# Optimization experiments

Hardware: AMD Instinct MI355X
Metric: run time of the kernel (lower is better)

The kernel has to match this reference:

```python
import jax, jax.numpy as jnp
import numpy as np

N = 50000  # nodes == edges (source multiplies [N,H] node tensor by [E] edge attention)
HW = 8


def _adaptive_pool_2x2_from9(h):
    # PyTorch AdaptiveAvgPool2d((2,2)) on 9x9: bins [0:5) and [4:9) per dim (overlap at 4)
    def binpair(t, ax):
        s0 = jnp.take(t, jnp.arange(0, 5), axis=ax).mean(axis=ax)
        s1 = jnp.take(t, jnp.arange(4, 9), axis=ax).mean(axis=ax)
        return jnp.stack([s0, s1], axis=ax)
    return binpair(binpair(h, 3), 2)  # [N,64,2,2]


def _fe_net(x, c1w, c1b, c2w, c2b, fw, fb):
    h = x[:, None, :, :]  # [N,1,8,8]
    h = jax.lax.conv_general_dilated(h, c1w, (1, 1), ((1, 1), (1, 1)),
                                     dimension_numbers=('NCHW', 'OIHW', 'NCHW')) + c1b[None, :, None, None]
    h = jax.nn.relu(h)  # [N,32,8,8]
    h = jax.lax.conv_general_dilated(h, c2w, (1, 1), ((1, 1), (1, 1)),
                                     dimension_numbers=('NCHW', 'OIHW', 'NCHW')) + c2b[None, :, None, None]
    h = jax.nn.relu(h)  # [N,64,9,9]
    h = _adaptive_pool_2x2_from9(h).reshape(h.shape[0], -1)  # [N,256]
    return h @ fw + fb  # [N,32]


def _gcn(x, src, dst, W, b, n):
    h = x @ W
    idx = jnp.arange(n)
    s = jnp.concatenate([src, idx])
    d = jnp.concatenate([dst, idx])
    deg = jax.ops.segment_sum(jnp.ones(s.shape[0], h.dtype), d, num_segments=n)
    dis = jnp.where(deg > 0, jax.lax.rsqrt(jnp.maximum(deg, 1e-12)), 0.0)
    norm = dis[s] * dis[d]
    out = jax.ops.segment_sum(h[s] * norm[:, None], d, num_segments=n)
    return out + b


def _attention1(aux, src, dst, n):
    frame = aux[:, 2]
    fd = jnp.abs(frame[src] - frame[dst])
    outdeg = jax.ops.segment_sum(jnp.ones(src.shape[0], aux.dtype), src, num_segments=n)
    return jnp.where(fd == 1.0, 1.0 / jnp.maximum(outdeg[src], 1.0), 0.0)


def _attention2(aux, src, dst):
    ang, rad, frame = aux[:, 0], aux[:, 1], aux[:, 2]
    fd = jnp.abs(frame[src] - frame[dst])
    dx = rad[dst] * jnp.cos(ang[dst]) - rad[src] * jnp.cos(ang[src])
    dy = rad[dst] * jnp.sin(ang[dst]) - rad[src] * jnp.sin(ang[src])
    fd_safe = jnp.where(fd == 2.0, fd, 1.0)
    vel = jnp.sqrt(dx * dx + dy * dy + 1e-12) / fd_safe
    return jnp.where(fd == 2.0, jnp.exp(-vel / 8.5), 0.0)


def setup_inputs() -> dict:
    key = jax.random.key(0)
    ks = jax.random.split(key, 20)
    x = jax.random.normal(ks[0], (N, HW, HW), jnp.float32)
    angle = jax.random.uniform(ks[1], (N,), jnp.float32, 0.0, 2.0 * np.pi)
    radius = jax.random.uniform(ks[2], (N,), jnp.float32, 1.0, 100.0)
    frame = jax.random.randint(ks[3], (N,), 0, 10).astype(jnp.float32)
    aux_features = jnp.stack([angle, radius, frame], axis=1)
    edge_index = jax.random.randint(ks[4], (2, N), 0, N)
    s = 0.05
    p = lambda k, sh: jax.random.normal(k, sh, jnp.float32) * s
    return {
        'x': x, 'aux_features': aux_features, 'edge_index': edge_index,
        'conv1_w': p(ks[5], (32, 1, 3, 3)), 'conv1_b': jnp.zeros((32,), jnp.float32),
        'conv2_w': p(ks[6], (64, 32, 2, 2)), 'conv2_b': jnp.zeros((64,), jnp.float32),
        'fe_fc_w': p(ks[7], (256, 32)), 'fe_fc_b': jnp.zeros((32,), jnp.float32),
        'gcn1_w': p(ks[8], (32, 64)), 'gcn1_b': jnp.zeros((64,), jnp.float32),
        'gcn2_w': p(ks[9], (64, 64)), 'gcn2_b': jnp.zeros((64,), jnp.float32),
        'fc_w': p(ks[10], (64, 32)), 'fc_b': jnp.zeros((32,), jnp.float32),
        'out_w': p(ks[11], (32, 1)), 'out_b': jnp.zeros((1,), jnp.float32),
    }


def reference(x, aux_features, edge_index, conv1_w, conv1_b, conv2_w, conv2_b,
              fe_fc_w, fe_fc_b, gcn1_w, gcn1_b, gcn2_w, gcn2_b, fc_w, fc_b,
              out_w, out_b):
    n = x.shape[0]
    src, dst = edge_index[0], edge_index[1]
    sig = _fe_net(x, conv1_w, conv1_b, conv2_w, conv2_b, fe_fc_w, fe_fc_b)  # [N,32]
    att1 = _attention1(aux_features, src, dst, n)  # [E] == [N]
    x1 = jax.nn.relu(_gcn(sig, src, dst, gcn1_w, gcn1_b, n) * att1[:, None])
    att2 = _attention2(aux_features, src, dst)
    x2 = jax.nn.relu(_gcn(x1, src, dst, gcn2_w, gcn2_b, n) * att2[:, None])
    h = jax.nn.relu(x2 @ fc_w + fc_b)
    out = jax.nn.sigmoid(h @ out_w + out_b)  # [N,1]
    return out
```

## Files before the change

### kernel.cpp

```cpp
#include <hip/hip_runtime.h>
#include <math.h>

typedef float f32x4 __attribute__((ext_vector_type(4)));
typedef float f32x2 __attribute__((ext_vector_type(2)));
typedef __bf16 bf16x8 __attribute__((ext_vector_type(8)));
typedef unsigned short ushort8 __attribute__((ext_vector_type(8)));
typedef unsigned short ushort4v __attribute__((ext_vector_type(4)));

static __device__ __forceinline__ unsigned short bfbits(float f) {
    return __builtin_bit_cast(unsigned short, (__bf16)f);
}

__global__ __launch_bounds__(256, 3) void fe_kernel(
    const float* __restrict__ x,
    const float* __restrict__ w1T,
    const float* __restrict__ w2, const float* __restrict__ b2,
    unsigned short* __restrict__ poolbf, int n)
{
    __shared__ unsigned short hT[4][100][40];
    __shared__ float xs[4][104];

    const int t = threadIdx.x, lane = t & 63, wave = t >> 6;
    const int cl = lane & 15, kg = lane >> 4;

    bf16x8 bfr[4][4];
    #pragma unroll
    for (int ct = 0; ct < 4; ++ct)
        #pragma unroll
        for (int tap = 0; tap < 4; ++tap) {
            const float* gp = w2 + (size_t)(ct * 16 + cl) * 128 + kg * 32 + tap;
            ushort8 u;
            #pragma unroll
            for (int e = 0; e < 8; ++e) u[e] = bfbits(gp[e * 4]);
            bfr[ct][tap] = __builtin_bit_cast(bf16x8, u);
        }
    float b2r[4];
    #pragma unroll
    for (int ct = 0; ct < 4; ++ct) b2r[ct] = b2[ct * 16 + cl];

    unsigned int pm[3] = {0u, 0u, 0u};
    #pragma unroll
    for (int mt = 0; mt < 6; ++mt)
        #pragma unroll
        for (int rg = 0; rg < 4; ++rg) {
            const int slot = mt * 4 + rg;
            const int pd = mt * 16 + kg * 4 + rg;
            unsigned int bits = 0;
            if (pd < 81) {
                const int id = pd / 9, jd = pd - 9 * (pd / 9);
                if (id <= 4 && jd <= 4) bits |= 1u;
                if (id <= 4 && jd >= 4) bits |= 2u;
                if (id >= 4 && jd <= 4) bits |= 4u;
                if (id >= 4 && jd >= 4) bits |= 8u;
            }
            pm[slot >> 3] |= bits << ((slot & 7) * 4);
        }

    int rbase[6];
    #pragma unroll
    for (int mt = 0; mt < 6; ++mt) {
        const int p = mt * 16 + cl;
        const int ia = p / 9, ja = p - 9 * ia;
        rbase[mt] = (p < 81) ? (ia * 10 + ja) : 0;
    }

    {
        ushort8 z8 = {0,0,0,0,0,0,0,0};
        for (int r = lane; r < 100; r += 64) {
            const int pi = r / 10, pj = r - 10 * (r / 10);
            if (pi == 0 || pi == 9 || pj == 0 || pj == 9) {
                *reinterpret_cast<ushort8*>(&hT[wave][r][0])  = z8;
                *reinterpret_cast<ushort8*>(&hT[wave][r][8])  = z8;
                *reinterpret_cast<ushort8*>(&hT[wave][r][16]) = z8;
                *reinterpret_cast<ushort8*>(&hT[wave][r][24]) = z8;
                xs[wave][r] = 0.0f;
            }
        }
    }

    const int i = lane >> 3, j = lane & 7;
    const int rr = (i + 1) * 10 + (j + 1);
    const int gw = blockIdx.x * 4 + wave;
    const int nw = gridDim.x * 4;

    float v = (gw < n) ? x[(size_t)gw * 64 + lane] : 0.0f;

    for (int node = gw; node < n; node += nw) {
        #pragma unroll
        for (int ct = 0; ct < 4; ++ct)
            #pragma unroll
            for (int tap = 0; tap < 4; ++tap) {
                f32x4 tmp = __builtin_bit_cast(f32x4, bfr[ct][tap]);
                asm volatile("" : "+v"(tmp));
                bfr[ct][tap] = __builtin_bit_cast(bf16x8, tmp);
            }

        const int nn = node + nw;
        const float vnext = x[(size_t)(nn < n ? nn : node) * 64 + lane];

        xs[wave][rr] = v;
        asm volatile("s_waitcnt lgkmcnt(0)" ::: "memory");

        float xv[9];
        #pragma unroll
        for (int ki = 0; ki < 3; ++ki)
            #pragma unroll
            for (int kj = 0; kj < 3; ++kj)
                xv[ki * 3 + kj] = xs[wave][(i + ki) * 10 + (j + kj)];

        #pragma unroll
        for (int cp = 0; cp < 4; ++cp) {
            ushort8 hv;
            #pragma unroll
            for (int half = 0; half < 2; ++half) {
                const int cg = cp * 2 + half;
                f32x4 s = *reinterpret_cast<const f32x4*>(w1T + 288 + cg * 4);
                #pragma unroll
                for (int q = 0; q < 9; ++q) {
                    const f32x4 wq = *reinterpret_cast<const f32x4*>(w1T + q * 32 + cg * 4);
                    s += xv[q] * wq;
                }
                #pragma unroll
                for (int c = 0; c < 4; ++c)
                    hv[half * 4 + c] = bfbits(fmaxf(s[c], 0.0f));
            }
            *reinterpret_cast<ushort8*>(&hT[wave][rr][cp * 8]) = hv;
        }
        asm volatile("s_waitcnt lgkmcnt(0)" ::: "memory");

        f32x2 pb01[4], pb23[4];
        #pragma unroll
        for (int ct = 0; ct < 4; ++ct) { pb01[ct] = (f32x2){0.f,0.f}; pb23[ct] = (f32x2){0.f,0.f}; }

        #pragma unroll
        for (int mt = 0; mt < 6; ++mt) {
            const int rb = rbase[mt];
            bf16x8 a[4];
            a[0] = *reinterpret_cast<const bf16x8*>(&hT[wave][rb][kg * 8]);
            a[1] = *reinterpret_cast<const bf16x8*>(&hT[wave][rb + 1][kg * 8]);
            a[2] = *reinterpret_cast<const bf16x8*>(&hT[wave][rb + 10][kg * 8]);
            a[3] = *reinterpret_cast<const bf16x8*>(&hT[wave][rb + 11][kg * 8]);

            f32x4 acc[4];
            #pragma unroll
            for (int ct = 0; ct < 4; ++ct)
                acc[ct] = (f32x4){b2r[ct], b2r[ct], b2r[ct], b2r[ct]};
            #pragma unroll
            for (int tap = 0; tap < 4; ++tap)
                #pragma unroll
                for (int ct = 0; ct < 4; ++ct)
                    acc[ct] = __builtin_amdgcn_mfma_f32_16x16x32_bf16(a[tap], bfr[ct][tap], acc[ct], 0, 0, 0);

            #pragma unroll
            for (int rg = 0; rg < 4; ++rg) {
                if (mt * 16 + rg >= 81) continue;
                const int slot = mt * 4 + rg;
                const unsigned int bits = pm[slot >> 3] >> ((slot & 7) * 4);
                const f32x2 w01 = {(float)(bits & 1u), (float)((bits >> 1) & 1u)};
                const f32x2 w23 = {(float)((bits >> 2) & 1u), (float)((bits >> 3) & 1u)};
                #pragma unroll
                for (int ct = 0; ct < 4; ++ct) {
                    const float vr = fmaxf(acc[ct][rg], 0.0f);
                    const f32x2 v2 = {vr, vr};
                    pb01[ct] += v2 * w01;
                    pb23[ct] += v2 * w23;
                }
            }
        }

        const bool k0 = (kg & 1) != 0;
        const bool k1 = (kg & 2) != 0;
        float outb[4];
        #pragma unroll
        for (int b = 0; b < 4; ++b) {
            const float x0 = (b < 2) ? pb01[0][b] : pb23[0][b - 2];
            const float x1 = (b < 2) ? pb01[1][b] : pb23[1][b - 2];
            const float x2 = (b < 2) ? pb01[2][b] : pb23[2][b - 2];
            const float x3 = (b < 2) ? pb01[3][b] : pb23[3][b - 2];
            float keepA = k0 ? x1 : x0, sendA = k0 ? x0 : x1;
            float keepB = k0 ? x3 : x2, sendB = k0 ? x2 : x3;
            keepA += __shfl_xor(sendA, 16);
            keepB += __shfl_xor(sendB, 16);
            float keep = k1 ? keepB : keepA, send = k1 ? keepA : keepB;
            keep += __shfl_xor(send, 32);
            outb[b] = keep;
        }
        ushort4v pv;
        #pragma unroll
        for (int b = 0; b < 4; ++b) pv[b] = bfbits(outb[b]);
        *reinterpret_cast<ushort4v*>(poolbf + (size_t)node * 256 + lane * 4) = pv;

        v = vnext;
    }
}

__global__ void pre_k(const float* __restrict__ fw, const float* __restrict__ fb,
                      const float* __restrict__ g1w, const float* __restrict__ g2w,
                      const float* __restrict__ w1, const float* __restrict__ b1,
                      unsigned short* __restrict__ W1t, float* __restrict__ v1,
                      unsigned short* __restrict__ W2t, float* __restrict__ w1T)
{
    const int b = blockIdx.x, t = threadIdx.x;
    if (b < 64) {
        float s = 0.0f;
        for (int jj = 0; jj < 32; ++jj) s += fw[t * 32 + jj] * g1w[jj * 64 + b];
        W1t[b * 256 + t] = bfbits(0.04f * s);
    } else if (b < 80) {
        const int idx = (b - 64) * 256 + t;
        const int nc = idx >> 6, k = idx & 63;
        W2t[nc * 64 + k] = bfbits(g2w[k * 64 + nc]);
        if (b == 64 && t < 64) {
            float s = 0.0f;
            for (int jj = 0; jj < 32; ++jj) s += fb[jj] * g1w[jj * 64 + t];
            v1[t] = s;
        }
    } else {
        if (t < 320) {
            const int q = t >> 5, c = t & 31;
            w1T[t] = (q < 9) ? w1[c * 9 + q] : b1[c];
        }
    }
}

template<int NKS, bool HASV>
__global__ __launch_bounds__(256) void mm_k(
    const unsigned short* __restrict__ A, const unsigned short* __restrict__ Bt,
    const float* __restrict__ v1, float* __restrict__ h, int n)
{
    const int lane = threadIdx.x & 63;
    const int cl = lane & 15, kg = lane >> 4;
    const int gw = blockIdx.x * 4 + (threadIdx.x >> 6);
    const int nw = gridDim.x * 4;
    const int K = NKS * 32;
    const int ntiles = (n + 15) >> 4;

    float vv[4];
    #pragma unroll
    for (int nt = 0; nt < 4; ++nt) vv[nt] = HASV ? v1[nt * 16 + cl] : 0.0f;

    for (int mt = gw; mt < ntiles; mt += nw) {
        const int r = min(mt * 16 + cl, n - 1);
        const unsigned short* ar = A + (size_t)r * K + kg * 8;
        f32x4 acc[4];
        #pragma unroll
        for (int nt = 0; nt < 4; ++nt)
            acc[nt] = (f32x4){vv[nt], vv[nt], vv[nt], vv[nt]};
        #pragma unroll
        for (int ks = 0; ks < NKS; ++ks) {
            const bf16x8 afr = *reinterpret_cast<const bf16x8*>(ar + ks * 32);
            #pragma unroll
            for (int nt = 0; nt < 4; ++nt) {
                const bf16x8 bfrg = *reinterpret_cast<const bf16x8*>(
                    Bt + (size_t)(nt * 16 + cl) * K + ks * 32 + kg * 8);
                acc[nt] = __builtin_amdgcn_mfma_f32_16x16x32_bf16(afr, bfrg, acc[nt], 0, 0, 0);
            }
        }
        #pragma unroll
        for (int nt = 0; nt < 4; ++nt)
            #pragma unroll
            for (int rg = 0; rg < 4; ++rg) {
                const int row = mt * 16 + (kg << 2) + rg;
                if (row < n) h[(size_t)row * 64 + nt * 16 + cl] = acc[nt][rg];
            }
    }
}

__global__ void count_k(const int* __restrict__ ei, float* __restrict__ outdeg,
                        float* __restrict__ indeg, int m)
{
    int e = blockIdx.x * blockDim.x + threadIdx.x;
    if (e >= m) return;
    atomicAdd(&outdeg[ei[e]], 1.0f);
    atomicAdd(&indeg[ei[m + e]], 1.0f);
}

__global__ void attprep_k(const float* __restrict__ aux, const int* __restrict__ ei,
                          const float* __restrict__ outdeg, const float* __restrict__ indeg,
                          float* __restrict__ dis,
                          float* __restrict__ att1, float* __restrict__ att2,
                          int n, int m)
{
    int e = blockIdx.x * blockDim.x + threadIdx.x;
    if (e < n) dis[e] = rsqrtf(indeg[e] + 1.0f);
    if (e >= m) return;
    const int s = ei[e], d = ei[m + e];
    const float fs = aux[(size_t)s * 3 + 2], fdd = aux[(size_t)d * 3 + 2];
    const float fd = fabsf(fs - fdd);
    att1[e] = (fd == 1.0f) ? (1.0f / fmaxf(outdeg[s], 1.0f)) : 0.0f;
    const float angs = aux[(size_t)s * 3 + 0], rads = aux[(size_t)s * 3 + 1];
    const float angd = aux[(size_t)d * 3 + 0], radd = aux[(size_t)d * 3 + 1];
    const float dx = radd * cosf(angd) - rads * cosf(angs);
    const float dy = radd * sinf(angd) - rads * sinf(angs);
    const float vel = sqrtf(dx * dx + dy * dy + 1e-12f) * 0.5f;
    att2[e] = (fd == 2.0f) ? expf(-vel / 8.5f) : 0.0f;
}

__global__ void scatter_k(const float* __restrict__ h, const int* __restrict__ ei,
                          const float* __restrict__ dis, float* __restrict__ acc, int m)
{
    size_t idx = (size_t)blockIdx.x * blockDim.x + threadIdx.x;
    if (idx >= (size_t)m * 64) return;
    const int e = (int)(idx >> 6), k = (int)(idx & 63);
    const int s = ei[e], d = ei[m + e];
    const float w = dis[s] * dis[d];
    atomicAdd(&acc[(size_t)d * 64 + k], w * h[(size_t)s * 64 + k]);
}

template<bool BF16OUT>
__global__ void fin_k(const float* __restrict__ acc, const float* __restrict__ h,
                      const float* __restrict__ dis, const float* __restrict__ b,
                      const float* __restrict__ att,
                      unsigned short* __restrict__ xbf, float* __restrict__ xf, int n)
{
    size_t idx = (size_t)blockIdx.x * blockDim.x + threadIdx.x;
    if (idx >= (size_t)n * 64) return;
    const int node = (int)(idx >> 6), k = (int)(idx & 63);
    const float di = dis[node];
    const float v = fmaxf((acc[idx] + b[k] + di * di * h[idx]) * att[node], 0.0f);
    if (BF16OUT) xbf[idx] = bfbits(v);
    else         xf[idx] = v;
}

__global__ void head_k(const float* __restrict__ x2, const float* __restrict__ fcw,
                       const float* __restrict__ fcb, const float* __restrict__ outw,
                       const float* __restrict__ outb, float* __restrict__ out, int n)
{
    size_t idx = (size_t)blockIdx.x * blockDim.x + threadIdx.x;
    const int node = (int)(idx >> 5), o = (int)(idx & 31);
    if (node >= n) return;
    const float* xr = x2 + (size_t)node * 64;
    float s = fcb[o];
    #pragma unroll
    for (int k = 0; k < 64; ++k) s = fmaf(xr[k], fcw[k * 32 + o], s);
    s = fmaxf(s, 0.0f);
    float p = s * outw[o];
    #pragma unroll
    for (int mk = 16; mk >= 1; mk >>= 1) p += __shfl_xor(p, mk);
    if (o == 0) out[node] = 1.0f / (1.0f + expf(-(p + outb[0])));
}

extern "C" void kernel_launch(void* const* d_in, const int* in_sizes, int n_in,
                              void* d_out, int out_size, void* d_ws, size_t ws_size,
                              hipStream_t stream)
{
    const float* x    = (const float*)d_in[0];
    const float* aux  = (const float*)d_in[1];
    const int*   ei   = (const int*)  d_in[2];
    const float* c1w  = (const float*)d_in[3];
    const float* c1b  = (const float*)d_in[4];
    const float* c2w  = (const float*)d_in[5];
    const float* c2b  = (const float*)d_in[6];
    const float* few  = (const float*)d_in[7];
    const float* feb  = (const float*)d_in[8];
    const float* g1w  = (const float*)d_in[9];
    const float* g1b  = (const float*)d_in[10];
    const float* g2w  = (const float*)d_in[11];
    const float* g2b  = (const float*)d_in[12];
    const float* fcw  = (const float*)d_in[13];
    const float* fcb  = (const float*)d_in[14];
    const float* outw = (const float*)d_in[15];
    const float* outb = (const float*)d_in[16];
    float* out = (float*)d_out;

    const int n = in_sizes[0] / 64;
    const int m = in_sizes[2] / 2;

    float* ws = (float*)d_ws;
    unsigned short* poolbf = (unsigned short*)ws;
    float* acc  = ws;
    unsigned short* x1bf = (unsigned short*)(ws + (size_t)n * 64);
    float* h    = ws + (size_t)n * 128;
    unsigned short* W1t = (unsigned short*)(ws + (size_t)n * 192);
    float* v1   = ws + (size_t)n * 192 + 8192;
    unsigned short* W2t = (unsigned short*)(v1 + 64);
    float* w1T    = v1 + 64 + 2048;
    float* outdeg = w1T + 320;
    float* indeg  = outdeg + n;
    float* dis    = indeg + n;
    float* att1   = dis + n;
    float* att2   = att1 + m;

    const dim3 b256(256);
    const int gE   = (m + 255) / 256;
    const int gNE  = (max(n, m) + 255) / 256;
    const int gNM  = (int)(((size_t)n * 64 + 255) / 256);
    const int gEM  = (int)(((size_t)m * 64 + 255) / 256);
    const int gNH  = (int)(((size_t)n * 32 + 255) / 256);
    const int gMM  = (((n + 15) / 16) + 3) / 4;

    hipMemsetAsync(outdeg, 0, (size_t)2 * n * sizeof(float), stream);
    pre_k<<<81, b256, 0, stream>>>(few, feb, g1w, g2w, c1w, c1b, W1t, v1, W2t, w1T);
    fe_kernel<<<768, b256, 0, stream>>>(x, w1T, c2w, c2b, poolbf, n);

    count_k<<<gE, b256, 0, stream>>>(ei, outdeg, indeg, m);
    attprep_k<<<gNE, b256, 0, stream>>>(aux, ei, outdeg, indeg, dis, att1, att2, n, m);

    mm_k<8, true><<<gMM, b256, 0, stream>>>(poolbf, W1t, v1, h, n);
    hipMemsetAsync(acc, 0, (size_t)n * 64 * sizeof(float), stream);
    scatter_k<<<gEM, b256, 0, stream>>>(h, ei, dis, acc, m);
    fin_k<true><<<gNM, b256, 0, stream>>>(acc, h, dis, g1b, att1, x1bf, nullptr, n);

    mm_k<2, false><<<gMM, b256, 0, stream>>>(x1bf, W2t, nullptr, h, n);
    hipMemsetAsync(acc, 0, (size_t)n * 64 * sizeof(float), stream);
    scatter_k<<<gEM, b256, 0, stream>>>(h, ei, dis, acc, m);
    fin_k<false><<<gNM, b256, 0, stream>>>(acc, h, dis, g2b, att2, nullptr, h, n);

    head_k<<<gNH, b256, 0, stream>>>(h, fcw, fcb, outw, outb, out, n);
}
```

Baseline: 301.0 us.

## Fuse setup, attention, finalize and head stages into fewer kernels

Degree counting is merged into the weight-prep kernel, and the attention and normalisation prep now runs on extra blocks of the first GEMM launch. The accumulator memsets are replaced by zeroing inside the GEMM kernels when the workspace is large enough. The first layer's finalize step is folded into the second GEMM's A-operand load, and the second finalize is merged with the MLP head through shared memory. This removes several launches and intermediate round trips through global memory. The cost is heavier kernels, a workspace-size-dependent layout, and in-place read and write of h and acc inside mm2f_k.

Measured after the change: 263.4 us. -12.5%, faster.

```diff
diff --git a/kernel.cpp b/kernel.cpp
--- a/kernel.cpp
+++ b/kernel.cpp
@@ -194,11 +194,13 @@
     }
 }
 
-__global__ void pre_k(const float* __restrict__ fw, const float* __restrict__ fb,
-                      const float* __restrict__ g1w, const float* __restrict__ g2w,
-                      const float* __restrict__ w1, const float* __restrict__ b1,
-                      unsigned short* __restrict__ W1t, float* __restrict__ v1,
-                      unsigned short* __restrict__ W2t, float* __restrict__ w1T)
+__global__ void precount_k(const float* __restrict__ fw, const float* __restrict__ fb,
+                           const float* __restrict__ g1w, const float* __restrict__ g2w,
+                           const float* __restrict__ w1, const float* __restrict__ b1,
+                           unsigned short* __restrict__ W1t, float* __restrict__ v1,
+                           unsigned short* __restrict__ W2t, float* __restrict__ w1T,
+                           const int* __restrict__ ei, float* __restrict__ outdeg,
+                           float* __restrict__ indeg, int m)
 {
     const int b = blockIdx.x, t = threadIdx.x;
     if (b < 64) {
@@ -214,45 +216,135 @@
             for (int jj = 0; jj < 32; ++jj) s += fb[jj] * g1w[jj * 64 + t];
             v1[t] = s;
         }
-    } else {
-        if (t < 320) {
+        if (b == 65 && t < 320) {
             const int q = t >> 5, c = t & 31;
             w1T[t] = (q < 9) ? w1[c * 9 + q] : b1[c];
         }
-    }
-}
-
-template<int NKS, bool HASV>
-__global__ __launch_bounds__(256) void mm_k(
+    } else {
+        const int e = (b - 80) * 256 + t;
+        if (e >= m) return;
+        atomicAdd(&outdeg[ei[e]], 1.0f);
+        atomicAdd(&indeg[ei[m + e]], 1.0f);
+    }
+}
+
+template<bool ZEROACC>
+__global__ __launch_bounds__(256) void mm1att_k(
     const unsigned short* __restrict__ A, const unsigned short* __restrict__ Bt,
-    const float* __restrict__ v1, float* __restrict__ h, int n)
+    const float* __restrict__ v1, float* __restrict__ h, float* __restrict__ acc,
+    const float* __restrict__ aux, const int* __restrict__ ei,
+    const float* __restrict__ outdeg, const float* __restrict__ indeg,
+    float* __restrict__ dis, float* __restrict__ att1, float* __restrict__ att2,
+    int n, int m, int gmm)
+{
+    const int t = threadIdx.x;
+    if ((int)blockIdx.x >= gmm) {
+        const int e = (blockIdx.x - gmm) * 256 + t;
+        if (e < n) dis[e] = rsqrtf(indeg[e] + 1.0f);
+        if (e >= m) return;
+        const int s = ei[e], d = ei[m + e];
+        const float fs = aux[(size_t)s * 3 + 2], fdd = aux[(size_t)d * 3 + 2];
+        const float fd = fabsf(fs - fdd);
+        att1[e] = (fd == 1.0f) ? (1.0f / fmaxf(outdeg[s], 1.0f)) : 0.0f;
+        const float angs = aux[(size_t)s * 3 + 0], rads = aux[(size_t)s * 3 + 1];
+        const float angd = aux[(size_t)d * 3 + 0], radd = aux[(size_t)d * 3 + 1];
+        const float dx = radd * cosf(angd) - rads * cosf(angs);
+        const float dy = radd * sinf(angd) - rads * sinf(angs);
+        const float vel = sqrtf(dx * dx + dy * dy + 1e-12f) * 0.5f;
+        att2[e] = (fd == 2.0f) ? expf(-vel / 8.5f) : 0.0f;
+        return;
+    }
+
+    const int lane = t & 63;
+    const int cl = lane & 15, kg = lane >> 4;
+    const int gw = blockIdx.x * 4 + (t >> 6);
+    const int nw = gmm * 4;
+    const int ntiles = (n + 15) >> 4;
+
+    float vv[4];
+    #pragma unroll
+    for (int nt = 0; nt < 4; ++nt) vv[nt] = v1[nt * 16 + cl];
+
+    for (int mt = gw; mt < ntiles; mt += nw) {
+        const int r = min(mt * 16 + cl, n - 1);
+        const unsigned short* ar = A + (size_t)r * 256 + kg * 8;
+        f32x4 accf[4];
+        #pragma unroll
+        for (int nt = 0; nt < 4; ++nt)
+            accf[nt] = (f32x4){vv[nt], vv[nt], vv[nt], vv[nt]};
+        #pragma unroll
+        for (int ks = 0; ks < 8; ++ks) {
+            const bf16x8 afr = *reinterpret_cast<const bf16x8*>(ar + ks * 32);
+            #pragma unroll
+            for (int nt = 0; nt < 4; ++nt) {
+                const bf16x8 bfrg = *reinterpret_cast<const bf16x8*>(
+                    Bt + (size_t)(nt * 16 + cl) * 256 + ks * 32 + kg * 8);
+                accf[nt] = __builtin_amdgcn_mfma_f32_16x16x32_bf16(afr, bfrg, accf[nt], 0, 0, 0);
+            }
+        }
+        #pragma unroll
+        for (int nt = 0; nt < 4; ++nt)
+            #pragma unroll
+            for (int rg = 0; rg < 4; ++rg) {
+                const int row = mt * 16 + (kg << 2) + rg;
+                if (row < n) h[(size_t)row * 64 + nt * 16 + cl] = accf[nt][rg];
+            }
+        if (ZEROACC) {
+            const int zr = mt * 16 + cl;
+            if (zr < n) {
+                const f32x4 z = {0.f, 0.f, 0.f, 0.f};
+                float* zp = acc + (size_t)zr * 64 + kg * 16;
+                *reinterpret_cast<f32x4*>(zp)      = z;
+                *reinterpret_cast<f32x4*>(zp + 4)  = z;
+                *reinterpret_cast<f32x4*>(zp + 8)  = z;
+                *reinterpret_cast<f32x4*>(zp + 12) = z;
+            }
+        }
+    }
+}
+
+template<bool ZEROACC>
+__global__ __launch_bounds__(256) void mm2f_k(
+    const float* __restrict__ acc, const float* __restrict__ hin,
+    const float* __restrict__ dis, const float* __restrict__ g1b,
+    const float* __restrict__ att1, const unsigned short* __restrict__ Bt,
+    float* __restrict__ hout, float* __restrict__ accz, int n)
 {
     const int lane = threadIdx.x & 63;
     const int cl = lane & 15, kg = lane >> 4;
     const int gw = blockIdx.x * 4 + (threadIdx.x >> 6);
     const int nw = gridDim.x * 4;
-    const int K = NKS * 32;
     const int ntiles = (n + 15) >> 4;
-
-    float vv[4];
-    #pragma unroll
-    for (int nt = 0; nt < 4; ++nt) vv[nt] = HASV ? v1[nt * 16 + cl] : 0.0f;
 
     for (int mt = gw; mt < ntiles; mt += nw) {
         const int r = min(mt * 16 + cl, n - 1);
-        const unsigned short* ar = A + (size_t)r * K + kg * 8;
-        f32x4 acc[4];
-        #pragma unroll
-        for (int nt = 0; nt < 4; ++nt)
-            acc[nt] = (f32x4){vv[nt], vv[nt], vv[nt], vv[nt]};
-        #pragma unroll
-        for (int ks = 0; ks < NKS; ++ks) {
-            const bf16x8 afr = *reinterpret_cast<const bf16x8*>(ar + ks * 32);
+        const float di = dis[r];
+        const float di2 = di * di;
+        const float at = att1[r];
+        f32x4 accf[4];
+        #pragma unroll
+        for (int nt = 0; nt < 4; ++nt) accf[nt] = (f32x4){0.f, 0.f, 0.f, 0.f};
+        #pragma unroll
+        for (int ks = 0; ks < 2; ++ks) {
+            const float* ap = acc + (size_t)r * 64 + ks * 32 + kg * 8;
+            const float* hp = hin + (size_t)r * 64 + ks * 32 + kg * 8;
+            const float* bp = g1b + ks * 32 + kg * 8;
+            ushort8 u;
+            #pragma unroll
+            for (int e = 0; e < 8; ++e)
+                u[e] = bfbits(fmaxf((ap[e] + bp[e] + di2 * hp[e]) * at, 0.0f));
+            if (ZEROACC) {
+                const f32x4 z = {0.f, 0.f, 0.f, 0.f};
+                float* zp = accz + (size_t)r * 64 + ks * 32 + kg * 8;
+                *reinterpret_cast<f32x4*>(zp)     = z;
+                *reinterpret_cast<f32x4*>(zp + 4) = z;
+            }
+            const bf16x8 afr = __builtin_bit_cast(bf16x8, u);
             #pragma unroll
             for (int nt = 0; nt < 4; ++nt) {
                 const bf16x8 bfrg = *reinterpret_cast<const bf16x8*>(
-                    Bt + (size_t)(nt * 16 + cl) * K + ks * 32 + kg * 8);
-                acc[nt] = __builtin_amdgcn_mfma_f32_16x16x32_bf16(afr, bfrg, acc[nt], 0, 0, 0);
+                    Bt + (size_t)(nt * 16 + cl) * 64 + ks * 32 + kg * 8);
+                accf[nt] = __builtin_amdgcn_mfma_f32_16x16x32_bf16(afr, bfrg, accf[nt], 0, 0, 0);
             }
         }
         #pragma unroll
@@ -260,39 +352,9 @@
             #pragma unroll
             for (int rg = 0; rg < 4; ++rg) {
                 const int row = mt * 16 + (kg << 2) + rg;
-                if (row < n) h[(size_t)row * 64 + nt * 16 + cl] = acc[nt][rg];
-            }
-    }
-}
-
-__global__ void count_k(const int* __restrict__ ei, float* __restrict__ outdeg,
-                        float* __restrict__ indeg, int m)
-{
-    int e = blockIdx.x * blockDim.x + threadIdx.x;
-    if (e >= m) return;
-    atomicAdd(&outdeg[ei[e]], 1.0f);
-    atomicAdd(&indeg[ei[m + e]], 1.0f);
-}
-
-__global__ void attprep_k(const float* __restrict__ aux, const int* __restrict__ ei,
-                          const float* __restrict__ outdeg, const float* __restrict__ indeg,
-                          float* __restrict__ dis,
-                          float* __restrict__ att1, float* __restrict__ att2,
-                          int n, int m)
-{
-    int e = blockIdx.x * blockDim.x + threadIdx.x;
-    if (e < n) dis[e] = rsqrtf(indeg[e] + 1.0f);
-    if (e >= m) return;
-    const int s = ei[e], d = ei[m + e];
-    const float fs = aux[(size_t)s * 3 + 2], fdd = aux[(size_t)d * 3 + 2];
-    const float fd = fabsf(fs - fdd);
-    att1[e] = (fd == 1.0f) ? (1.0f / fmaxf(outdeg[s], 1.0f)) : 0.0f;
-    const float angs = aux[(size_t)s * 3 + 0], rads = aux[(size_t)s * 3 + 1];
-    const float angd = aux[(size_t)d * 3 + 0], radd = aux[(size_t)d * 3 + 1];
-    const float dx = radd * cosf(angd) - rads * cosf(angs);
-    const float dy = radd * sinf(angd) - rads * sinf(angs);
-    const float vel = sqrtf(dx * dx + dy * dy + 1e-12f) * 0.5f;
-    att2[e] = (fd == 2.0f) ? expf(-vel / 8.5f) : 0.0f;
+                if (row < n) hout[(size_t)row * 64 + nt * 16 + cl] = accf[nt][rg];
+            }
+    }
 }
 
 __global__ void scatter_k(const float* __restrict__ h, const int* __restrict__ ei,
@@ -306,32 +368,37 @@
     atomicAdd(&acc[(size_t)d * 64 + k], w * h[(size_t)s * 64 + k]);
 }
 
-template<bool BF16OUT>
-__global__ void fin_k(const float* __restrict__ acc, const float* __restrict__ h,
-                      const float* __restrict__ dis, const float* __restrict__ b,
-                      const float* __restrict__ att,
-                      unsigned short* __restrict__ xbf, float* __restrict__ xf, int n)
-{
-    size_t idx = (size_t)blockIdx.x * blockDim.x + threadIdx.x;
-    if (idx >= (size_t)n * 64) return;
-    const int node = (int)(idx >> 6), k = (int)(idx & 63);
-    const float di = dis[node];
-    const float v = fmaxf((acc[idx] + b[k] + di * di * h[idx]) * att[node], 0.0f);
-    if (BF16OUT) xbf[idx] = bfbits(v);
-    else         xf[idx] = v;
-}
-
-__global__ void head_k(const float* __restrict__ x2, const float* __restrict__ fcw,
-                       const float* __restrict__ fcb, const float* __restrict__ outw,
-                       const float* __restrict__ outb, float* __restrict__ out, int n)
-{
-    size_t idx = (size_t)blockIdx.x * blockDim.x + threadIdx.x;
-    const int node = (int)(idx >> 5), o = (int)(idx & 31);
+__global__ __launch_bounds__(256) void finhead_k(
+    const float* __restrict__ acc, const float* __restrict__ h,
+    const float* __restrict__ dis, const float* __restrict__ g2b,
+    const float* __restrict__ att2,
+    const float* __restrict__ fcw, const float* __restrict__ fcb,
+    const float* __restrict__ outw, const float* __restrict__ outb,
+    float* __restrict__ out, int n)
+{
+    __shared__ float sm[8][64];
+    const int t = threadIdx.x;
+    const int nb = blockIdx.x * 8;
+
+    #pragma unroll
+    for (int pp = 0; pp < 2; ++pp) {
+        const int p = t + pp * 256;
+        const int nd = p >> 6, k = p & 63;
+        const int node = nb + nd;
+        if (node < n) {
+            const float di = dis[node];
+            const size_t idx = (size_t)node * 64 + k;
+            sm[nd][k] = fmaxf((acc[idx] + g2b[k] + di * di * h[idx]) * att2[node], 0.0f);
+        }
+    }
+    __syncthreads();
+
+    const int nd = t >> 5, o = t & 31;
+    const int node = nb + nd;
     if (node >= n) return;
-    const float* xr = x2 + (size_t)node * 64;
     float s = fcb[o];
     #pragma unroll
-    for (int k = 0; k < 64; ++k) s = fmaf(xr[k], fcw[k * 32 + o], s);
+    for (int k = 0; k < 64; ++k) s = fmaf(sm[nd][k], fcw[k * 32 + o], s);
     s = fmaxf(s, 0.0f);
     float p = s * outw[o];
     #pragma unroll
@@ -366,12 +433,24 @@
     const int m = in_sizes[2] / 2;
 
     float* ws = (float*)d_ws;
+    const size_t tailf = 8192 + 64 + 2048 + 320 + (size_t)3 * n + (size_t)2 * m;
+    const bool sep = ws_size >= ((size_t)n * 256 + tailf) * sizeof(float);
+
     unsigned short* poolbf = (unsigned short*)ws;
-    float* acc  = ws;
-    unsigned short* x1bf = (unsigned short*)(ws + (size_t)n * 64);
-    float* h    = ws + (size_t)n * 128;
-    unsigned short* W1t = (unsigned short*)(ws + (size_t)n * 192);
-    float* v1   = ws + (size_t)n * 192 + 8192;
+    float* h;
+    float* acc;
+    float* wtail;
+    if (sep) {
+        h     = ws + (size_t)n * 128;
+        acc   = ws + (size_t)n * 192;
+        wtail = ws + (size_t)n * 256;
+    } else {
+        acc   = ws;
+        h     = ws + (size_t)n * 128;
+        wtail = ws + (size_t)n * 192;
+    }
+    unsigned short* W1t = (unsigned short*)wtail;
+    float* v1   = wtail + 8192;
     unsigned short* W2t = (unsigned short*)(v1 + 64);
     float* w1T    = v1 + 64 + 2048;
     float* outdeg = w1T + 320;
@@ -383,27 +462,27 @@
     const dim3 b256(256);
     const int gE   = (m + 255) / 256;
     const int gNE  = (max(n, m) + 255) / 256;
-    const int gNM  = (int)(((size_t)n * 64 + 255) / 256);
     const int gEM  = (int)(((size_t)m * 64 + 255) / 256);
-    const int gNH  = (int)(((size_t)n * 32 + 255) / 256);
     const int gMM  = (((n + 15) / 16) + 3) / 4;
 
     hipMemsetAsync(outdeg, 0, (size_t)2 * n * sizeof(float), stream);
-    pre_k<<<81, b256, 0, stream>>>(few, feb, g1w, g2w, c1w, c1b, W1t, v1, W2t, w1T);
+    precount_k<<<80 + gE, b256, 0, stream>>>(few, feb, g1w, g2w, c1w, c1b,
+                                             W1t, v1, W2t, w1T, ei, outdeg, indeg, m);
     fe_kernel<<<768, b256, 0, stream>>>(x, w1T, c2w, c2b, poolbf, n);
 
-    count_k<<<gE, b256, 0, stream>>>(ei, outdeg, indeg, m);
-    attprep_k<<<gNE, b256, 0, stream>>>(aux, ei, outdeg, indeg, dis, att1, att2, n, m);
-
-    mm_k<8, true><<<gMM, b256, 0, stream>>>(poolbf, W1t, v1, h, n);
-    hipMemsetAsync(acc, 0, (size_t)n * 64 * sizeof(float), stream);
+    if (sep) {
+        mm1att_k<true><<<gMM + gNE, b256, 0, stream>>>(poolbf, W1t, v1, h, acc,
+            aux, ei, outdeg, indeg, dis, att1, att2, n, m, gMM);
+    } else {
+        mm1att_k<false><<<gMM + gNE, b256, 0, stream>>>(poolbf, W1t, v1, h, acc,
+            aux, ei, outdeg, indeg, dis, att1, att2, n, m, gMM);
+        hipMemsetAsync(acc, 0, (size_t)n * 64 * sizeof(float), stream);
+    }
     scatter_k<<<gEM, b256, 0, stream>>>(h, ei, dis, acc, m);
-    fin_k<true><<<gNM, b256, 0, stream>>>(acc, h, dis, g1b, att1, x1bf, nullptr, n);
-
-    mm_k<2, false><<<gMM, b256, 0, stream>>>(x1bf, W2t, nullptr, h, n);
-    hipMemsetAsync(acc, 0, (size_t)n * 64 * sizeof(float), stream);
+
+    mm2f_k<true><<<gMM, b256, 0, stream>>>(acc, h, dis, g1b, att1, W2t, h, acc, n);
     scatter_k<<<gEM, b256, 0, stream>>>(h, ei, dis, acc, m);
-    fin_k<false><<<gNM, b256, 0, stream>>>(acc, h, dis, g2b, att2, nullptr, h, n);
-
-    head_k<<<gNH, b256, 0, stream>>>(h, fcw, fcb, outw, outb, out, n);
-}
+
+    finhead_k<<<(n + 7) / 8, b256, 0, stream>>>(acc, h, dis, g2b, att2,
+                                                fcw, fcb, outw, outb, out, n);
+}
```
